# Performance work log

Hardware: AMD Instinct MI355X
Metric: run time of the kernel (lower is better)

## Reference

```python
import jax, jax.numpy as jnp
import numpy as np

N_NODES = 50000
N_EDGES = 800000
N_FEAT = 128
HIDDEN = 256
BN_EPS = 1e-5


def setup_inputs() -> dict:
    key = jax.random.key(0)
    ks = jax.random.split(key, 8)
    x = jax.random.normal(ks[0], (N_NODES, N_FEAT), dtype=jnp.float32)
    edge_index = jax.random.randint(ks[1], (2, N_EDGES), 0, N_NODES, dtype=jnp.int64)
    # Xavier-uniform linear weights (as in weights_init), zero biases
    def xavier(k, fan_in, fan_out):
        lim = float(np.sqrt(6.0 / (fan_in + fan_out)))
        return jax.random.uniform(k, (fan_in, fan_out), jnp.float32, -lim, lim)
    return {
        "x": x,
        "edge_index": edge_index,
        "W1": xavier(ks[2], N_FEAT, HIDDEN),
        "b1": jnp.zeros((HIDDEN,), jnp.float32),
        "g1": jnp.ones((HIDDEN,), jnp.float32),
        "be1": jnp.zeros((HIDDEN,), jnp.float32),
        "W2": xavier(ks[3], HIDDEN, HIDDEN),
        "b2": jnp.zeros((HIDDEN,), jnp.float32),
        "g2": jnp.ones((HIDDEN,), jnp.float32),
        "be2": jnp.zeros((HIDDEN,), jnp.float32),
        "Wfc": xavier(ks[4], HIDDEN, HIDDEN),
        "bfc": jnp.zeros((HIDDEN,), jnp.float32),
    }


def gcn_conv(x, src, dst, deg_inv_sqrt, W, b):
    """PyG GCNConv: out_i = sum_{j->i} d_i^-1/2 d_j^-1/2 (x_j W) + b,
    with self-loops already appended to (src, dst)."""
    h = x @ W                                        # [N, out]
    norm = deg_inv_sqrt[src] * deg_inv_sqrt[dst]     # [E+N]
    msgs = h[src] * norm[:, None]                    # gather + scale
    out = jax.ops.segment_sum(msgs, dst, num_segments=x.shape[0])
    return out + b


def batch_norm(x, gamma, beta):
    # training-mode BatchNorm1d: batch stats over nodes, biased variance
    mean = jnp.mean(x, axis=0)
    var = jnp.mean(jnp.square(x - mean), axis=0)
    return (x - mean) * jax.lax.rsqrt(var + BN_EPS) * gamma + beta


def reference(x, edge_index, W1, b1, g1, be1, W2, b2, g2, be2, Wfc, bfc):
    n = x.shape[0]
    loop = jnp.arange(n, dtype=edge_index.dtype)
    src = jnp.concatenate([edge_index[0], loop])
    dst = jnp.concatenate([edge_index[1], loop])
    deg = jax.ops.segment_sum(jnp.ones_like(src, dtype=x.dtype), dst, num_segments=n)
    deg_inv_sqrt = jnp.where(deg > 0, jax.lax.rsqrt(jnp.maximum(deg, 1.0)), 0.0)

    h = gcn_conv(x, src, dst, deg_inv_sqrt, W1, b1)
    h = batch_norm(h, g1, be1)
    # dropout is identity in deterministic (eval) reference
    h = gcn_conv(h, src, dst, deg_inv_sqrt, W2, b2)
    h = batch_norm(h, g2, be2)
    return h @ Wfc + bfc
```

## Files before the change

### kernel.cpp

```cpp
#include <hip/hip_runtime.h>
#include <hip/hip_bf16.h>

#define NFEAT 128
#define HID 256
#define BN_EPS 1e-5f
#define NBIN 64

typedef __attribute__((ext_vector_type(8))) __bf16 bf16x8;
typedef __attribute__((ext_vector_type(4))) float f32x4;

static __device__ __forceinline__ float bflo(unsigned u) {
    union { unsigned x; float f; } c; c.x = u << 16; return c.f;
}
static __device__ __forceinline__ float bfhi(unsigned u) {
    union { unsigned x; float f; } c; c.x = u & 0xffff0000u; return c.f;
}

__global__ void k_count(const int* __restrict__ ei, int E, int* __restrict__ cnt,
                        int* __restrict__ rank) {
    int e = blockIdx.x * blockDim.x + threadIdx.x;
    if (e < E) rank[e] = atomicAdd(&cnt[ei[E + e]], 1);
}

__global__ void k_scan1(const int* __restrict__ cnt, int n, int* __restrict__ partial,
                        int* __restrict__ blk_total) {
    __shared__ int sh[256];
    int i = blockIdx.x * 256 + threadIdx.x;
    int v = (i < n) ? cnt[i] : 0;
    sh[threadIdx.x] = v;
    __syncthreads();
    for (int off = 1; off < 256; off <<= 1) {
        int x = (threadIdx.x >= off) ? sh[threadIdx.x - off] : 0;
        __syncthreads();
        sh[threadIdx.x] += x;
        __syncthreads();
    }
    if (i < n) partial[i] = sh[threadIdx.x] - v;
    if (threadIdx.x == 255) blk_total[blockIdx.x] = sh[255];
}

__global__ void k_scan2(int* __restrict__ blk, int nb) {
    __shared__ int sh[256];
    int t = threadIdx.x;
    int v = (t < nb) ? blk[t] : 0;
    sh[t] = v;
    __syncthreads();
    for (int off = 1; off < 256; off <<= 1) {
        int x = (t >= off) ? sh[t - off] : 0;
        __syncthreads();
        sh[t] += x;
        __syncthreads();
    }
    if (t < nb) blk[t] = sh[t] - v;
}

__global__ void k_finalize(const int* __restrict__ partial, const int* __restrict__ blk,
                           const int* __restrict__ cnt, int n, int* __restrict__ row_start,
                           float* __restrict__ dinv) {
    int i = blockIdx.x * blockDim.x + threadIdx.x;
    if (i < n) {
        row_start[i] = partial[i] + blk[i >> 8];
        dinv[i] = rsqrtf((float)(cnt[i] + 1));
    }
}

__global__ void k_fill(const int* __restrict__ ei, const int* __restrict__ rank,
                       const int* __restrict__ row_start, int E, int* __restrict__ col) {
    int e = blockIdx.x * blockDim.x + threadIdx.x;
    if (e < E) {
        int d = ei[E + e];
        col[row_start[d] + rank[e]] = ei[e];
    }
}

__global__ __launch_bounds__(256) void k_rvec(const int* __restrict__ rs,
                                              const int* __restrict__ rc,
                                              const int* __restrict__ col,
                                              const float* __restrict__ dinv,
                                              float* __restrict__ r, int N) {
    const int wid = blockIdx.x * 4 + (threadIdx.x >> 6);
    if (wid >= N) return;
    const int lane = threadIdx.x & 63;
    const int s = rs[wid];
    const int deg = rc[wid];
    float acc = 0.f;
    for (int e = lane; e < deg; e += 64) acc += dinv[col[s + e]];
#pragma unroll
    for (int m = 1; m < 64; m <<= 1) acc += __shfl_xor(acc, m);
    if (lane == 0) {
        float di = dinv[wid];
        r[wid] = di * (di + acc);
    }
}

__global__ void k_scale_cast(const float* __restrict__ in, const float* __restrict__ dinv,
                             __hip_bfloat16* __restrict__ out, int shift, int n4) {
    int i = blockIdx.x * blockDim.x + threadIdx.x;
    if (i < n4) {
        float d = dinv[i >> shift];
        float4 v = *(const float4*)(in + (size_t)i * 4);
        __hip_bfloat16* o = out + (size_t)i * 4;
        o[0] = __float2bfloat16(v.x * d);
        o[1] = __float2bfloat16(v.y * d);
        o[2] = __float2bfloat16(v.z * d);
        o[3] = __float2bfloat16(v.w * d);
    }
}

__global__ void k_transpose2(const float* __restrict__ W1, const float* __restrict__ Wf,
                             __hip_bfloat16* __restrict__ Wt1, __hip_bfloat16* __restrict__ Wtf) {
    int idx = blockIdx.x * 256 + threadIdx.x;
    if (idx < 32768) {
        int n = idx & 255;
        int k = idx >> 8;
        Wt1[n * 128 + k] = __float2bfloat16(W1[k * 256 + n]);
    } else {
        int base = idx - 32768;
        int n = base & 255;
        int k = base >> 8;
        Wtf[n * 256 + k] = __float2bfloat16(Wf[k * 256 + n]);
    }
}

__global__ void k_bnfold(const float* __restrict__ gs, const float* __restrict__ g,
                         const float* __restrict__ be, const float* __restrict__ b, float invN,
                         float* __restrict__ sc, float* __restrict__ bv) {
    int c = threadIdx.x;
    float s = 0.f, q = 0.f;
    for (int r = 0; r < NBIN; r++) {
        s += gs[r * 512 + c];
        q += gs[r * 512 + 256 + c];
    }
    float mean = s * invN;
    float var = q * invN - mean * mean;
    float scl = rsqrtf(var + BN_EPS) * g[c];
    float bb = b ? b[c] : 0.f;
    sc[c] = scl;
    bv[c] = (bb - mean) * scl + be[c];
}

__global__ __launch_bounds__(256) void k_foldW(const float* __restrict__ W1,
                                               const float* __restrict__ W2,
                                               const float* __restrict__ sc,
                                               __hip_bfloat16* __restrict__ WfT) {
    int k = blockIdx.x;
    int n = threadIdx.x;
    float acc = 0.f;
    for (int m = 0; m < 256; m++) acc += W1[k * 256 + m] * sc[m] * W2[m * 256 + n];
    WfT[(size_t)n * 128 + k] = __float2bfloat16(acc);
}

__global__ void k_uvec(const float* __restrict__ W2, const float* __restrict__ bv,
                       float* __restrict__ u) {
    int n = threadIdx.x;
    float acc = 0.f;
    for (int m = 0; m < 256; m++) acc += W2[m * 256 + n] * bv[m];
    u[n] = acc;
}

template <int PL>
static __device__ __forceinline__ void loadrow(const __hip_bfloat16* p, float* v) {
    if constexpr (PL == 4) {
        uint2 u = *(const uint2*)p;
        v[0] = bflo(u.x); v[1] = bfhi(u.x); v[2] = bflo(u.y); v[3] = bfhi(u.y);
    } else {
        unsigned u = *(const unsigned*)p;
        v[0] = bflo(u); v[1] = bfhi(u);
    }
}

template <int C>
__global__ __launch_bounds__(256) void k_spmm_w(const __hip_bfloat16* __restrict__ Hs,
                                                const int* __restrict__ rs,
                                                const int* __restrict__ rc,
                                                const int* __restrict__ col,
                                                const float* __restrict__ dinv,
                                                __hip_bfloat16* __restrict__ out,
                                                __hip_bfloat16* __restrict__ out2, int N) {
    constexpr int PL = C / 64;
    const int wid = blockIdx.x * 4 + (threadIdx.x >> 6);
    if (wid >= N) return;
    const int lane = threadIdx.x & 63;
    const int ch = lane * PL;
    const int s = rs[wid];
    const int deg = rc[wid];
    const float di = dinv[wid];

    float acc[PL];
    loadrow<PL>(Hs + (size_t)wid * C + ch, acc);

    int e = 0;
    for (; e + 8 <= deg; e += 8) {
        int idx[8];
#pragma unroll
        for (int j = 0; j < 8; j++) idx[j] = col[s + e + j];
        float v[8][PL];
#pragma unroll
        for (int j = 0; j < 8; j++) loadrow<PL>(Hs + (size_t)idx[j] * C + ch, v[j]);
#pragma unroll
        for (int j = 0; j < 8; j++)
#pragma unroll
            for (int i = 0; i < PL; i++) acc[i] += v[j][i];
    }
    for (; e < deg; e++) {
        int i0 = col[s + e];
        float v0[PL];
        loadrow<PL>(Hs + (size_t)i0 * C + ch, v0);
#pragma unroll
        for (int i = 0; i < PL; i++) acc[i] += v0[i];
    }
    union { unsigned u[PL / 2]; unsigned short us[PL]; } o;
#pragma unroll
    for (int i = 0; i < PL; i++) {
        __hip_bfloat16 b = __float2bfloat16(di * acc[i]);
        o.us[i] = *(unsigned short*)&b;
    }
    if constexpr (PL == 4)
        *(uint2*)(out + (size_t)wid * C + ch) = *(uint2*)o.u;
    else
        *(unsigned*)(out + (size_t)wid * C + ch) = o.u[0];
    if (out2) {
        union { unsigned u[PL / 2]; unsigned short us[PL]; } o2;
        float d2 = di * di;
#pragma unroll
        for (int i = 0; i < PL; i++) {
            __hip_bfloat16 b = __float2bfloat16(d2 * acc[i]);
            o2.us[i] = *(unsigned short*)&b;
        }
        if constexpr (PL == 4)
            *(uint2*)(out2 + (size_t)wid * C + ch) = *(uint2*)o2.u;
        else
            *(unsigned*)(out2 + (size_t)wid * C + ch) = o2.u[0];
    }
}

template <int K, bool STATS>
__global__ __launch_bounds__(256, 4) void k_gemm2(const __hip_bfloat16* __restrict__ A,
                                                  const __hip_bfloat16* __restrict__ Bt,
                                                  const float* __restrict__ bias,
                                                  __hip_bfloat16* __restrict__ outb,
                                                  float* __restrict__ outf,
                                                  float* __restrict__ gs,
                                                  const float* __restrict__ rvec,
                                                  const float* __restrict__ uvec,
                                                  const float* __restrict__ bnsc,
                                                  const float* __restrict__ bnof, int M) {
    constexpr int NC = K / 64;
    constexpr int LDR = 72;
    __shared__ __align__(16) unsigned short Bs[2 * 128 * LDR];
    float* sred = (float*)Bs;
    float* qred = sred + 512;

    const int t = threadIdx.x;
    const int wv = t >> 6;
    const int lane = t & 63;
    const int mlane = lane & 15;
    const int quad = lane >> 4;
    const int m0 = blockIdx.x * 128;
    const int n0 = blockIdx.y * 128;
    const int arow0 = m0 + wv * 32 + mlane;

    auto stage = [&](int c, int buf) {
#pragma unroll
        for (int i = 0; i < 4; i++) {
            int idx = t + i * 256;
            int row = idx >> 3;
            int c4 = idx & 7;
            uint4 v = *(const uint4*)(Bt + (size_t)(n0 + row) * K + c * 64 + c4 * 8);
            *(uint4*)(Bs + buf * (128 * LDR) + row * LDR + c4 * 8) = v;
        }
    };
    auto loadA = [&](int c, bf16x8 (&dst)[2][2]) {
#pragma unroll
        for (int mt = 0; mt < 2; mt++)
#pragma unroll
            for (int ks = 0; ks < 2; ks++) {
                int cb = c * 64 + ks * 32 + quad * 8;
                bf16x8 raw = *(const bf16x8*)(A + (size_t)(arow0 + mt * 16) * K + cb);
                if (bnsc) {
                    union { bf16x8 v; unsigned u[4]; } cu; cu.v = raw;
                    union { unsigned u[4]; unsigned short us[8]; } ou;
#pragma unroll
                    for (int j = 0; j < 4; j++) {
                        float lo = bflo(cu.u[j]) * bnsc[cb + 2 * j] + bnof[cb + 2 * j];
                        float hi = bfhi(cu.u[j]) * bnsc[cb + 2 * j + 1] + bnof[cb + 2 * j + 1];
                        __hip_bfloat16 bl = __float2bfloat16(lo);
                        __hip_bfloat16 bh = __float2bfloat16(hi);
                        ou.us[2 * j] = *(unsigned short*)&bl;
                        ou.us[2 * j + 1] = *(unsigned short*)&bh;
                    }
                    dst[mt][ks] = *(bf16x8*)ou.u;
                } else {
                    dst[mt][ks] = raw;
                }
            }
    };

    f32x4 acc[2][8];
#pragma unroll
    for (int mt = 0; mt < 2; mt++)
#pragma unroll
        for (int i = 0; i < 8; i++) acc[mt][i] = (f32x4){0.f, 0.f, 0.f, 0.f};

    bf16x8 aP[2][2], aQ[2][2];
    loadA(0, aP);
    stage(0, 0);

    auto mmachunk = [&](int c, bf16x8 (&ac)[2][2]) {
        const unsigned short* base = Bs + (c & 1) * (128 * LDR);
#pragma unroll
        for (int nt = 0; nt < 8; nt++) {
            const unsigned short* bp = base + (nt * 16 + mlane) * LDR + quad * 8;
#pragma unroll
            for (int ks = 0; ks < 2; ks++) {
                bf16x8 b = *(const bf16x8*)(bp + ks * 32);
                acc[0][nt] = __builtin_amdgcn_mfma_f32_16x16x32_bf16(ac[0][ks], b, acc[0][nt], 0, 0, 0);
                acc[1][nt] = __builtin_amdgcn_mfma_f32_16x16x32_bf16(ac[1][ks], b, acc[1][nt], 0, 0, 0);
            }
        }
    };

#pragma unroll
    for (int c = 0; c < NC; c++) {
        __syncthreads();
        if (c + 1 < NC) {
            stage(c + 1, (c + 1) & 1);
            if ((c & 1) == 0) loadA(c + 1, aQ); else loadA(c + 1, aP);
        }
        if ((c & 1) == 0) mmachunk(c, aP); else mmachunk(c, aQ);
    }

    float rv[2][4] = {{0.f, 0.f, 0.f, 0.f}, {0.f, 0.f, 0.f, 0.f}};
    if (rvec) {
#pragma unroll
        for (int mt = 0; mt < 2; mt++)
#pragma unroll
            for (int r = 0; r < 4; r++) {
                int row = m0 + wv * 32 + mt * 16 + quad * 4 + r;
                if (row < M) rv[mt][r] = rvec[row];
            }
    }
    float sp[8], qp[8];
#pragma unroll
    for (int nt = 0; nt < 8; nt++) {
        int colx = n0 + nt * 16 + mlane;
        float bv = bias[colx];
        float uvn = uvec ? uvec[colx] : 0.f;
        float s = 0.f, q = 0.f;
#pragma unroll
        for (int mt = 0; mt < 2; mt++)
#pragma unroll
            for (int r = 0; r < 4; r++) {
                int row = m0 + wv * 32 + mt * 16 + quad * 4 + r;
                if (row < M) {
                    float h = acc[mt][nt][r] + bv + rv[mt][r] * uvn;
                    if (outb) outb[(size_t)row * HID + colx] = __float2bfloat16(h);
                    if (outf) outf[(size_t)row * HID + colx] = h;
                    s += h;
                    q += h * h;
                }
            }
        sp[nt] = s;
        qp[nt] = q;
    }
    if constexpr (STATS) {
#pragma unroll
        for (int nt = 0; nt < 8; nt++) {
            sp[nt] += __shfl_xor(sp[nt], 16);
            sp[nt] += __shfl_xor(sp[nt], 32);
            qp[nt] += __shfl_xor(qp[nt], 16);
            qp[nt] += __shfl_xor(qp[nt], 32);
        }
        __syncthreads();
        if (quad == 0) {
#pragma unroll
            for (int nt = 0; nt < 8; nt++) {
                sred[wv * 128 + nt * 16 + mlane] = sp[nt];
                qred[wv * 128 + nt * 16 + mlane] = qp[nt];
            }
        }
        __syncthreads();
        if (t < 128) {
            float ss = sred[t] + sred[128 + t] + sred[256 + t] + sred[384 + t];
            float qq = qred[t] + qred[128 + t] + qred[256 + t] + qred[384 + t];
            float* bin = gs + (blockIdx.x & (NBIN - 1)) * 512;
            atomicAdd(&bin[n0 + t], ss);
            atomicAdd(&bin[256 + n0 + t], qq);
        }
    }
}

extern "C" void kernel_launch(void* const* d_in, const int* in_sizes, int n_in, void* d_out,
                              int out_size, void* d_ws, size_t ws_size, hipStream_t stream) {
    const float* x = (const float*)d_in[0];
    const int* ei = (const int*)d_in[1];
    const float* W1 = (const float*)d_in[2];
    const float* b1 = (const float*)d_in[3];
    const float* g1 = (const float*)d_in[4];
    const float* be1 = (const float*)d_in[5];
    const float* W2 = (const float*)d_in[6];
    const float* b2 = (const float*)d_in[7];
    const float* g2 = (const float*)d_in[8];
    const float* be2 = (const float*)d_in[9];
    const float* Wfc = (const float*)d_in[10];
    const float* bfc = (const float*)d_in[11];
    float* out = (float*)d_out;

    const int N = in_sizes[0] / NFEAT;
    const int E = in_sizes[1] / 2;
    const float invN = 1.0f / (float)N;

    char* ws = (char*)d_ws;
    size_t off = 0;
    auto alloc = [&](size_t bytes) -> void* {
        void* p = ws + off;
        off += (bytes + 255) & ~(size_t)255;
        return p;
    };
    int* row_cnt = (int*)alloc((size_t)N * 4);
    int* partial = (int*)alloc((size_t)N * 4);
    int* row_start = (int*)alloc((size_t)N * 4);
    int* blk = (int*)alloc(256 * 4);
    float* dinv = (float*)alloc((size_t)N * 4);
    int* rank = (int*)alloc((size_t)E * 4);
    int* col_idx = (int*)alloc((size_t)E * 4);
    float* gs1 = (float*)alloc((size_t)NBIN * 512 * 4);
    float* gs2 = (float*)alloc((size_t)NBIN * 512 * 4);
    float* sc1 = (float*)alloc(256 * 4);
    float* bv1 = (float*)alloc(256 * 4);
    float* uvec = (float*)alloc(256 * 4);
    float* sc2 = (float*)alloc(256 * 4);
    float* of2 = (float*)alloc(256 * 4);
    float* rvec = (float*)alloc((size_t)(N + 128) * 4);
    __hip_bfloat16* Wt1 = (__hip_bfloat16*)alloc(256 * 128 * 2);
    __hip_bfloat16* Wtf = (__hip_bfloat16*)alloc(256 * 256 * 2);
    __hip_bfloat16* WfT = (__hip_bfloat16*)alloc(256 * 128 * 2);
    __hip_bfloat16* xs = (__hip_bfloat16*)alloc((size_t)(N + 128) * NFEAT * 2);
    __hip_bfloat16* aggX = (__hip_bfloat16*)alloc((size_t)(N + 128) * NFEAT * 2);
    __hip_bfloat16* t1s = (__hip_bfloat16*)alloc((size_t)(N + 128) * NFEAT * 2);
    __hip_bfloat16* h2 = (__hip_bfloat16*)alloc((size_t)(N + 128) * HID * 2);
    __hip_bfloat16* t2 = xs;

    hipMemsetAsync(row_cnt, 0, (size_t)N * 4, stream);
    hipMemsetAsync(gs1, 0, (size_t)NBIN * 512 * 4 * 2, stream);

    k_count<<<(E + 255) / 256, 256, 0, stream>>>(ei, E, row_cnt, rank);
    int nblk = (N + 255) / 256;
    k_scan1<<<nblk, 256, 0, stream>>>(row_cnt, N, partial, blk);
    k_scan2<<<1, 256, 0, stream>>>(blk, nblk);
    k_finalize<<<nblk, 256, 0, stream>>>(partial, blk, row_cnt, N, row_start, dinv);
    k_fill<<<(E + 255) / 256, 256, 0, stream>>>(ei, rank, row_start, E, col_idx);

    k_transpose2<<<384, 256, 0, stream>>>(W1, Wfc, Wt1, Wtf);

    k_scale_cast<<<(N * NFEAT / 4 + 255) / 256, 256, 0, stream>>>(x, dinv, xs, 5, N * NFEAT / 4);

    int sg = (N + 3) / 4;
    k_rvec<<<sg, 256, 0, stream>>>(row_start, row_cnt, col_idx, dinv, rvec, N);

    dim3 gg((N + 127) / 128, 2);
    k_spmm_w<NFEAT><<<sg, 256, 0, stream>>>(xs, row_start, row_cnt, col_idx, dinv, aggX, t1s, N);
    k_gemm2<NFEAT, true><<<gg, 256, 0, stream>>>(aggX, Wt1, b1, nullptr, nullptr, gs1,
                                                 nullptr, nullptr, nullptr, nullptr, N);
    k_bnfold<<<1, 256, 0, stream>>>(gs1, g1, be1, b1, invN, sc1, bv1);
    k_foldW<<<128, 256, 0, stream>>>(W1, W2, sc1, WfT);
    k_uvec<<<1, 256, 0, stream>>>(W2, bv1, uvec);
    k_spmm_w<NFEAT><<<sg, 256, 0, stream>>>(t1s, row_start, row_cnt, col_idx, dinv, t2, nullptr, N);
    k_gemm2<NFEAT, true><<<gg, 256, 0, stream>>>(t2, WfT, b2, h2, nullptr, gs2,
                                                 rvec, uvec, nullptr, nullptr, N);
    k_bnfold<<<1, 256, 0, stream>>>(gs2, g2, be2, nullptr, invN, sc2, of2);
    k_gemm2<HID, false><<<gg, 256, 0, stream>>>(h2, Wtf, bfc, nullptr, out, nullptr,
                                                nullptr, nullptr, sc2, of2, N);
}
```

Before: 347.6 us.

## Fuse small prep kernels, fold final BN into Wfc, merge rvec into SpMM

Several small launches are merged: the block-scan second pass is folded into finalize, the cast and W1 transpose share one kernel, and BN fold, W fold and u-vector are computed in one kernel. The final BatchNorm is folded into the Wfc weights and bias, so the last GEMM no longer applies a per-element scale and offset on its A operand. The rvec computation moves into the first SpMM, and the second SpMM now applies the dinv scaling on the fly. This removes the extra t1s output, a separate pass over the edges, and per-load BN arithmetic. The cost is an extra per-edge dinv gather inside the SpMM loops.

```diff
diff --git a/kernel.cpp b/kernel.cpp
--- a/kernel.cpp
+++ b/kernel.cpp
@@ -39,27 +39,21 @@
     if (threadIdx.x == 255) blk_total[blockIdx.x] = sh[255];
 }
 
-__global__ void k_scan2(int* __restrict__ blk, int nb) {
-    __shared__ int sh[256];
-    int t = threadIdx.x;
-    int v = (t < nb) ? blk[t] : 0;
-    sh[t] = v;
+__global__ void k_finalize(const int* __restrict__ partial, const int* __restrict__ blk_total,
+                           const int* __restrict__ cnt, int n, int nblk,
+                           int* __restrict__ row_start, float* __restrict__ dinv) {
+    __shared__ int sw[4];
+    const int t = threadIdx.x;
+    const int b = blockIdx.x;
+    int v = (t < b && t < nblk) ? blk_total[t] : 0;
+#pragma unroll
+    for (int m = 1; m < 64; m <<= 1) v += __shfl_xor(v, m);
+    if ((t & 63) == 0) sw[t >> 6] = v;
     __syncthreads();
-    for (int off = 1; off < 256; off <<= 1) {
-        int x = (t >= off) ? sh[t - off] : 0;
-        __syncthreads();
-        sh[t] += x;
-        __syncthreads();
-    }
-    if (t < nb) blk[t] = sh[t] - v;
-}
-
-__global__ void k_finalize(const int* __restrict__ partial, const int* __restrict__ blk,
-                           const int* __restrict__ cnt, int n, int* __restrict__ row_start,
-                           float* __restrict__ dinv) {
-    int i = blockIdx.x * blockDim.x + threadIdx.x;
+    int pref = sw[0] + sw[1] + sw[2] + sw[3];
+    int i = b * 256 + t;
     if (i < n) {
-        row_start[i] = partial[i] + blk[i >> 8];
+        row_start[i] = partial[i] + pref;
         dinv[i] = rsqrtf((float)(cnt[i] + 1));
     }
 }
@@ -73,59 +67,40 @@
     }
 }
 
-__global__ __launch_bounds__(256) void k_rvec(const int* __restrict__ rs,
-                                              const int* __restrict__ rc,
-                                              const int* __restrict__ col,
-                                              const float* __restrict__ dinv,
-                                              float* __restrict__ r, int N) {
-    const int wid = blockIdx.x * 4 + (threadIdx.x >> 6);
-    if (wid >= N) return;
-    const int lane = threadIdx.x & 63;
-    const int s = rs[wid];
-    const int deg = rc[wid];
-    float acc = 0.f;
-    for (int e = lane; e < deg; e += 64) acc += dinv[col[s + e]];
-#pragma unroll
-    for (int m = 1; m < 64; m <<= 1) acc += __shfl_xor(acc, m);
-    if (lane == 0) {
-        float di = dinv[wid];
-        r[wid] = di * (di + acc);
-    }
-}
-
-__global__ void k_scale_cast(const float* __restrict__ in, const float* __restrict__ dinv,
-                             __hip_bfloat16* __restrict__ out, int shift, int n4) {
-    int i = blockIdx.x * blockDim.x + threadIdx.x;
-    if (i < n4) {
-        float d = dinv[i >> shift];
-        float4 v = *(const float4*)(in + (size_t)i * 4);
-        __hip_bfloat16* o = out + (size_t)i * 4;
-        o[0] = __float2bfloat16(v.x * d);
-        o[1] = __float2bfloat16(v.y * d);
-        o[2] = __float2bfloat16(v.z * d);
-        o[3] = __float2bfloat16(v.w * d);
-    }
-}
-
-__global__ void k_transpose2(const float* __restrict__ W1, const float* __restrict__ Wf,
-                             __hip_bfloat16* __restrict__ Wt1, __hip_bfloat16* __restrict__ Wtf) {
-    int idx = blockIdx.x * 256 + threadIdx.x;
-    if (idx < 32768) {
+__global__ void k_prep(const float* __restrict__ x, const float* __restrict__ dinv,
+                       __hip_bfloat16* __restrict__ xs, const float* __restrict__ W1,
+                       __hip_bfloat16* __restrict__ Wt1, int castBlocks, int n4) {
+    int bid = blockIdx.x;
+    int t = threadIdx.x;
+    if (bid < castBlocks) {
+        int i = bid * 256 + t;
+        if (i < n4) {
+            float d = dinv[i >> 5];
+            float4 v = *(const float4*)(x + (size_t)i * 4);
+            __hip_bfloat16* o = xs + (size_t)i * 4;
+            o[0] = __float2bfloat16(v.x * d);
+            o[1] = __float2bfloat16(v.y * d);
+            o[2] = __float2bfloat16(v.z * d);
+            o[3] = __float2bfloat16(v.w * d);
+        }
+    } else {
+        int idx = (bid - castBlocks) * 256 + t;
         int n = idx & 255;
         int k = idx >> 8;
         Wt1[n * 128 + k] = __float2bfloat16(W1[k * 256 + n]);
-    } else {
-        int base = idx - 32768;
-        int n = base & 255;
-        int k = base >> 8;
-        Wtf[n * 256 + k] = __float2bfloat16(Wf[k * 256 + n]);
-    }
-}
-
-__global__ void k_bnfold(const float* __restrict__ gs, const float* __restrict__ g,
-                         const float* __restrict__ be, const float* __restrict__ b, float invN,
-                         float* __restrict__ sc, float* __restrict__ bv) {
-    int c = threadIdx.x;
+    }
+}
+
+__global__ __launch_bounds__(256) void k_bnfoldW(const float* __restrict__ gs,
+                                                 const float* __restrict__ g,
+                                                 const float* __restrict__ be,
+                                                 const float* __restrict__ b, float invN,
+                                                 const float* __restrict__ W1,
+                                                 const float* __restrict__ W2,
+                                                 __hip_bfloat16* __restrict__ WfT,
+                                                 float* __restrict__ uvec) {
+    __shared__ float shs[256], shb[256];
+    const int c = threadIdx.x;
     float s = 0.f, q = 0.f;
     for (int r = 0; r < NBIN; r++) {
         s += gs[r * 512 + c];
@@ -134,104 +109,101 @@
     float mean = s * invN;
     float var = q * invN - mean * mean;
     float scl = rsqrtf(var + BN_EPS) * g[c];
-    float bb = b ? b[c] : 0.f;
-    sc[c] = scl;
-    bv[c] = (bb - mean) * scl + be[c];
-}
-
-__global__ __launch_bounds__(256) void k_foldW(const float* __restrict__ W1,
-                                               const float* __restrict__ W2,
-                                               const float* __restrict__ sc,
-                                               __hip_bfloat16* __restrict__ WfT) {
-    int k = blockIdx.x;
-    int n = threadIdx.x;
-    float acc = 0.f;
-    for (int m = 0; m < 256; m++) acc += W1[k * 256 + m] * sc[m] * W2[m * 256 + n];
-    WfT[(size_t)n * 128 + k] = __float2bfloat16(acc);
-}
-
-__global__ void k_uvec(const float* __restrict__ W2, const float* __restrict__ bv,
-                       float* __restrict__ u) {
-    int n = threadIdx.x;
-    float acc = 0.f;
-    for (int m = 0; m < 256; m++) acc += W2[m * 256 + n] * bv[m];
-    u[n] = acc;
-}
-
-template <int PL>
-static __device__ __forceinline__ void loadrow(const __hip_bfloat16* p, float* v) {
-    if constexpr (PL == 4) {
-        uint2 u = *(const uint2*)p;
-        v[0] = bflo(u.x); v[1] = bfhi(u.x); v[2] = bflo(u.y); v[3] = bfhi(u.y);
+    shs[c] = scl;
+    shb[c] = (b[c] - mean) * scl + be[c];
+    __syncthreads();
+    if (blockIdx.x < 128) {
+        int k = blockIdx.x;
+        float acc = 0.f;
+        for (int m = 0; m < 256; m++) acc += W1[k * 256 + m] * shs[m] * W2[m * 256 + c];
+        WfT[(size_t)c * 128 + k] = __float2bfloat16(acc);
     } else {
-        unsigned u = *(const unsigned*)p;
-        v[0] = bflo(u); v[1] = bfhi(u);
-    }
-}
-
-template <int C>
-__global__ __launch_bounds__(256) void k_spmm_w(const __hip_bfloat16* __restrict__ Hs,
-                                                const int* __restrict__ rs,
-                                                const int* __restrict__ rc,
-                                                const int* __restrict__ col,
-                                                const float* __restrict__ dinv,
-                                                __hip_bfloat16* __restrict__ out,
-                                                __hip_bfloat16* __restrict__ out2, int N) {
-    constexpr int PL = C / 64;
+        float acc = 0.f;
+        for (int m = 0; m < 256; m++) acc += W2[m * 256 + c] * shb[m];
+        uvec[c] = acc;
+    }
+}
+
+__global__ __launch_bounds__(256) void k_fold2(const float* __restrict__ gs,
+                                               const float* __restrict__ g,
+                                               const float* __restrict__ be, float invN,
+                                               const float* __restrict__ Wfc,
+                                               const float* __restrict__ bfc,
+                                               __hip_bfloat16* __restrict__ Wtf,
+                                               float* __restrict__ bias2) {
+    __shared__ float shs[256], sho[256];
+    const int c = threadIdx.x;
+    float s = 0.f, q = 0.f;
+    for (int r = 0; r < NBIN; r++) {
+        s += gs[r * 512 + c];
+        q += gs[r * 512 + 256 + c];
+    }
+    float mean = s * invN;
+    float var = q * invN - mean * mean;
+    float scl = rsqrtf(var + BN_EPS) * g[c];
+    shs[c] = scl;
+    sho[c] = (0.f - mean) * scl + be[c];
+    __syncthreads();
+    if (blockIdx.x < 256) {
+        int k = blockIdx.x;
+        Wtf[(size_t)c * 256 + k] = __float2bfloat16(Wfc[k * 256 + c] * shs[k]);
+    } else {
+        float acc = bfc[c];
+        for (int m = 0; m < 256; m++) acc += sho[m] * Wfc[m * 256 + c];
+        bias2[c] = acc;
+    }
+}
+
+template <bool SCALE>
+__global__ __launch_bounds__(256) void k_spmm(const __hip_bfloat16* __restrict__ Hs,
+                                              const int* __restrict__ rs,
+                                              const int* __restrict__ rc,
+                                              const int* __restrict__ col,
+                                              const float* __restrict__ dinv,
+                                              __hip_bfloat16* __restrict__ out,
+                                              float* __restrict__ rv, int N) {
     const int wid = blockIdx.x * 4 + (threadIdx.x >> 6);
     if (wid >= N) return;
     const int lane = threadIdx.x & 63;
-    const int ch = lane * PL;
+    const int ch = lane * 2;
     const int s = rs[wid];
     const int deg = rc[wid];
     const float di = dinv[wid];
 
-    float acc[PL];
-    loadrow<PL>(Hs + (size_t)wid * C + ch, acc);
+    unsigned u0 = *(const unsigned*)(Hs + (size_t)wid * 128 + ch);
+    float a0, a1, dsum = 0.f;
+    if constexpr (SCALE) { a0 = di * bflo(u0); a1 = di * bfhi(u0); }
+    else { a0 = bflo(u0); a1 = bfhi(u0); }
 
     int e = 0;
     for (; e + 8 <= deg; e += 8) {
         int idx[8];
 #pragma unroll
         for (int j = 0; j < 8; j++) idx[j] = col[s + e + j];
-        float v[8][PL];
-#pragma unroll
-        for (int j = 0; j < 8; j++) loadrow<PL>(Hs + (size_t)idx[j] * C + ch, v[j]);
-#pragma unroll
-        for (int j = 0; j < 8; j++)
-#pragma unroll
-            for (int i = 0; i < PL; i++) acc[i] += v[j][i];
+        float dj[8];
+#pragma unroll
+        for (int j = 0; j < 8; j++) dj[j] = dinv[idx[j]];
+        unsigned u[8];
+#pragma unroll
+        for (int j = 0; j < 8; j++) u[j] = *(const unsigned*)(Hs + (size_t)idx[j] * 128 + ch);
+#pragma unroll
+        for (int j = 0; j < 8; j++) {
+            if constexpr (SCALE) { a0 += dj[j] * bflo(u[j]); a1 += dj[j] * bfhi(u[j]); }
+            else { a0 += bflo(u[j]); a1 += bfhi(u[j]); dsum += dj[j]; }
+        }
     }
     for (; e < deg; e++) {
         int i0 = col[s + e];
-        float v0[PL];
-        loadrow<PL>(Hs + (size_t)i0 * C + ch, v0);
-#pragma unroll
-        for (int i = 0; i < PL; i++) acc[i] += v0[i];
-    }
-    union { unsigned u[PL / 2]; unsigned short us[PL]; } o;
-#pragma unroll
-    for (int i = 0; i < PL; i++) {
-        __hip_bfloat16 b = __float2bfloat16(di * acc[i]);
-        o.us[i] = *(unsigned short*)&b;
-    }
-    if constexpr (PL == 4)
-        *(uint2*)(out + (size_t)wid * C + ch) = *(uint2*)o.u;
-    else
-        *(unsigned*)(out + (size_t)wid * C + ch) = o.u[0];
-    if (out2) {
-        union { unsigned u[PL / 2]; unsigned short us[PL]; } o2;
-        float d2 = di * di;
-#pragma unroll
-        for (int i = 0; i < PL; i++) {
-            __hip_bfloat16 b = __float2bfloat16(d2 * acc[i]);
-            o2.us[i] = *(unsigned short*)&b;
-        }
-        if constexpr (PL == 4)
-            *(uint2*)(out2 + (size_t)wid * C + ch) = *(uint2*)o2.u;
-        else
-            *(unsigned*)(out2 + (size_t)wid * C + ch) = o2.u[0];
-    }
+        float d0 = dinv[i0];
+        unsigned uu = *(const unsigned*)(Hs + (size_t)i0 * 128 + ch);
+        if constexpr (SCALE) { a0 += d0 * bflo(uu); a1 += d0 * bfhi(uu); }
+        else { a0 += bflo(uu); a1 += bfhi(uu); dsum += d0; }
+    }
+    union { unsigned w; unsigned short us[2]; } o;
+    __hip_bfloat16 b0 = __float2bfloat16(di * a0); o.us[0] = *(unsigned short*)&b0;
+    __hip_bfloat16 b1 = __float2bfloat16(di * a1); o.us[1] = *(unsigned short*)&b1;
+    *(unsigned*)(out + (size_t)wid * 128 + ch) = o.w;
+    if (!SCALE && rv && lane == 0) rv[wid] = di * (di + dsum);
 }
 
 template <int K, bool STATS>
@@ -242,9 +214,7 @@
                                                   float* __restrict__ outf,
                                                   float* __restrict__ gs,
                                                   const float* __restrict__ rvec,
-                                                  const float* __restrict__ uvec,
-                                                  const float* __restrict__ bnsc,
-                                                  const float* __restrict__ bnof, int M) {
+                                                  const float* __restrict__ uvec, int M) {
     constexpr int NC = K / 64;
     constexpr int LDR = 72;
     __shared__ __align__(16) unsigned short Bs[2 * 128 * LDR];
@@ -274,26 +244,9 @@
 #pragma unroll
         for (int mt = 0; mt < 2; mt++)
 #pragma unroll
-            for (int ks = 0; ks < 2; ks++) {
-                int cb = c * 64 + ks * 32 + quad * 8;
-                bf16x8 raw = *(const bf16x8*)(A + (size_t)(arow0 + mt * 16) * K + cb);
-                if (bnsc) {
-                    union { bf16x8 v; unsigned u[4]; } cu; cu.v = raw;
-                    union { unsigned u[4]; unsigned short us[8]; } ou;
-#pragma unroll
-                    for (int j = 0; j < 4; j++) {
-                        float lo = bflo(cu.u[j]) * bnsc[cb + 2 * j] + bnof[cb + 2 * j];
-                        float hi = bfhi(cu.u[j]) * bnsc[cb + 2 * j + 1] + bnof[cb + 2 * j + 1];
-                        __hip_bfloat16 bl = __float2bfloat16(lo);
-                        __hip_bfloat16 bh = __float2bfloat16(hi);
-                        ou.us[2 * j] = *(unsigned short*)&bl;
-                        ou.us[2 * j + 1] = *(unsigned short*)&bh;
-                    }
-                    dst[mt][ks] = *(bf16x8*)ou.u;
-                } else {
-                    dst[mt][ks] = raw;
-                }
-            }
+            for (int ks = 0; ks < 2; ks++)
+                dst[mt][ks] = *(const bf16x8*)(A + (size_t)(arow0 + mt * 16) * K + c * 64 +
+                                               ks * 32 + quad * 8);
     };
 
     f32x4 acc[2][8];
@@ -418,57 +371,47 @@
         return p;
     };
     int* row_cnt = (int*)alloc((size_t)N * 4);
+    float* gs1 = (float*)alloc((size_t)NBIN * 512 * 4);
+    float* gs2 = (float*)alloc((size_t)NBIN * 512 * 4);
+    size_t zero_bytes = ((size_t)ws - (size_t)row_cnt) + off;
     int* partial = (int*)alloc((size_t)N * 4);
     int* row_start = (int*)alloc((size_t)N * 4);
     int* blk = (int*)alloc(256 * 4);
     float* dinv = (float*)alloc((size_t)N * 4);
     int* rank = (int*)alloc((size_t)E * 4);
     int* col_idx = (int*)alloc((size_t)E * 4);
-    float* gs1 = (float*)alloc((size_t)NBIN * 512 * 4);
-    float* gs2 = (float*)alloc((size_t)NBIN * 512 * 4);
-    float* sc1 = (float*)alloc(256 * 4);
-    float* bv1 = (float*)alloc(256 * 4);
     float* uvec = (float*)alloc(256 * 4);
-    float* sc2 = (float*)alloc(256 * 4);
-    float* of2 = (float*)alloc(256 * 4);
+    float* bias2 = (float*)alloc(256 * 4);
     float* rvec = (float*)alloc((size_t)(N + 128) * 4);
     __hip_bfloat16* Wt1 = (__hip_bfloat16*)alloc(256 * 128 * 2);
     __hip_bfloat16* Wtf = (__hip_bfloat16*)alloc(256 * 256 * 2);
     __hip_bfloat16* WfT = (__hip_bfloat16*)alloc(256 * 128 * 2);
     __hip_bfloat16* xs = (__hip_bfloat16*)alloc((size_t)(N + 128) * NFEAT * 2);
     __hip_bfloat16* aggX = (__hip_bfloat16*)alloc((size_t)(N + 128) * NFEAT * 2);
-    __hip_bfloat16* t1s = (__hip_bfloat16*)alloc((size_t)(N + 128) * NFEAT * 2);
     __hip_bfloat16* h2 = (__hip_bfloat16*)alloc((size_t)(N + 128) * HID * 2);
     __hip_bfloat16* t2 = xs;
 
-    hipMemsetAsync(row_cnt, 0, (size_t)N * 4, stream);
-    hipMemsetAsync(gs1, 0, (size_t)NBIN * 512 * 4 * 2, stream);
+    hipMemsetAsync(row_cnt, 0, zero_bytes, stream);
 
     k_count<<<(E + 255) / 256, 256, 0, stream>>>(ei, E, row_cnt, rank);
     int nblk = (N + 255) / 256;
     k_scan1<<<nblk, 256, 0, stream>>>(row_cnt, N, partial, blk);
-    k_scan2<<<1, 256, 0, stream>>>(blk, nblk);
-    k_finalize<<<nblk, 256, 0, stream>>>(partial, blk, row_cnt, N, row_start, dinv);
+    k_finalize<<<nblk, 256, 0, stream>>>(partial, blk, row_cnt, N, nblk, row_start, dinv);
     k_fill<<<(E + 255) / 256, 256, 0, stream>>>(ei, rank, row_start, E, col_idx);
 
-    k_transpose2<<<384, 256, 0, stream>>>(W1, Wfc, Wt1, Wtf);
-
-    k_scale_cast<<<(N * NFEAT / 4 + 255) / 256, 256, 0, stream>>>(x, dinv, xs, 5, N * NFEAT / 4);
+    int castBlocks = (N * NFEAT / 4 + 255) / 256;
+    k_prep<<<castBlocks + 128, 256, 0, stream>>>(x, dinv, xs, W1, Wt1, castBlocks, N * NFEAT / 4);
 
     int sg = (N + 3) / 4;
-    k_rvec<<<sg, 256, 0, stream>>>(row_start, row_cnt, col_idx, dinv, rvec, N);
-
     dim3 gg((N + 127) / 128, 2);
-    k_spmm_w<NFEAT><<<sg, 256, 0, stream>>>(xs, row_start, row_cnt, col_idx, dinv, aggX, t1s, N);
+    k_spmm<false><<<sg, 256, 0, stream>>>(xs, row_start, row_cnt, col_idx, dinv, aggX, rvec, N);
+    k_spmm<true><<<sg, 256, 0, stream>>>(aggX, row_start, row_cnt, col_idx, dinv, t2, nullptr, N);
     k_gemm2<NFEAT, true><<<gg, 256, 0, stream>>>(aggX, Wt1, b1, nullptr, nullptr, gs1,
-                                                 nullptr, nullptr, nullptr, nullptr, N);
-    k_bnfold<<<1, 256, 0, stream>>>(gs1, g1, be1, b1, invN, sc1, bv1);
-    k_foldW<<<128, 256, 0, stream>>>(W1, W2, sc1, WfT);
-    k_uvec<<<1, 256, 0, stream>>>(W2, bv1, uvec);
-    k_spmm_w<NFEAT><<<sg, 256, 0, stream>>>(t1s, row_start, row_cnt, col_idx, dinv, t2, nullptr, N);
+                                                 nullptr, nullptr, N);
+    k_bnfoldW<<<129, 256, 0, stream>>>(gs1, g1, be1, b1, invN, W1, W2, WfT, uvec);
     k_gemm2<NFEAT, true><<<gg, 256, 0, stream>>>(t2, WfT, b2, h2, nullptr, gs2,
-                                                 rvec, uvec, nullptr, nullptr, N);
-    k_bnfold<<<1, 256, 0, stream>>>(gs2, g2, be2, nullptr, invN, sc2, of2);
-    k_gemm2<HID, false><<<gg, 256, 0, stream>>>(h2, Wtf, bfc, nullptr, out, nullptr,
-                                                nullptr, nullptr, sc2, of2, N);
-}
+                                                 rvec, uvec, N);
+    k_fold2<<<257, 256, 0, stream>>>(gs2, g2, be2, invN, Wfc, bfc, Wtf, bias2);
+    k_gemm2<HID, false><<<gg, 256, 0, stream>>>(h2, Wtf, bias2, nullptr, out, nullptr,
+                                                nullptr, nullptr, N);
+}
```

Result: faster. 317.4 us (-8.7%).
